# Kernel optimization log

Measured on AMD Instinct MI355X. Metric: run time of the kernel, lower is better.

Reference implementation:

```python
import jax, jax.numpy as jnp
import numpy as np

B, S, D = 2, 2048, 1024
H = 16
HD = D // H  # 64
SCALE = HD ** 0.5


def setup_inputs() -> dict:
    key = jax.random.key(0)
    ks = jax.random.split(key, 7)
    return {
        "query": jax.random.normal(ks[0], (B, S, D), dtype=jnp.float32),
        "key": jax.random.normal(ks[1], (B, S, D), dtype=jnp.float32),
        "value": jax.random.normal(ks[2], (B, S, D), dtype=jnp.float32),
        "W_qkv_w": jax.random.normal(ks[3], (3 * D, 3 * D), dtype=jnp.float32) * (1.0 / np.sqrt(3 * D)),
        "W_qkv_b": jax.random.normal(ks[4], (3 * D,), dtype=jnp.float32) * 0.02,
        "W_o_w": jax.random.normal(ks[5], (D, D), dtype=jnp.float32) * (1.0 / np.sqrt(D)),
        "W_o_b": jax.random.normal(ks[6], (D,), dtype=jnp.float32) * 0.02,
    }


def _split_heads(x):
    # [B,S,D] -> [B,H,S,HD]
    return x.reshape(B, S, H, HD).transpose(0, 2, 1, 3)


def reference(query, key, value, W_qkv_w, W_qkv_b, W_o_w, W_o_b):
    # fused QKV projection: concat then Linear(3D, 3D)  (torch: x @ W.T + b)
    qkv = jnp.concatenate([query, key, value], axis=-1)
    qkv = qkv @ W_qkv_w.T + W_qkv_b
    q, k, v = jnp.split(qkv, 3, axis=-1)
    q, k, v = _split_heads(q), _split_heads(k), _split_heads(v)
    # naive attention: materializes [B,H,S,S]
    scores = jnp.einsum('bhqd,bhkd->bhqk', q, k) / SCALE
    probs = jax.nn.softmax(scores, axis=-1)
    attn = jnp.einsum('bhqk,bhkd->bhqd', probs, v)
    # combine heads: [B,H,S,HD] -> [B,S,D]
    attn = attn.transpose(0, 2, 1, 3).reshape(B, S, D)
    return attn @ W_o_w.T + W_o_b
```

## Files before the change

kernel.cpp:

```cpp
#include <hip/hip_runtime.h>
#include <cmath>

#define BS   2
#define SEQ  2048
#define DM   1024
#define NH   16
#define HD   64
#define D3   3072
#define MROWS 4096
#define KVBLK 64
#define QBLK  128
#define NTILES (SEQ / KVBLK)

#define CSC 0.18033688011112042f

typedef _Float16 f16;
typedef __attribute__((ext_vector_type(4))) _Float16 half4;
typedef __attribute__((ext_vector_type(8))) _Float16 half8;
typedef __attribute__((ext_vector_type(4))) float f32x4;
typedef unsigned int u32;
typedef __attribute__((ext_vector_type(2))) u32 u32x2;
typedef __attribute__((ext_vector_type(4))) u32 u32x4;

__device__ __forceinline__ void async_cp16(const void* g, void* s) {
    __builtin_amdgcn_global_load_lds(
        (const __attribute__((address_space(1))) u32*)g,
        (__attribute__((address_space(3))) u32*)s, 16, 0, 0);
}

__global__ __launch_bounds__(256) void conv_concat_kernel(
    const float* __restrict__ q, const float* __restrict__ k,
    const float* __restrict__ v, f16* __restrict__ out)
{
    const int seg = blockIdx.x;
    const int row = blockIdx.y;
    const int c   = threadIdx.x * 4;
    const float* src = (seg == 0 ? q : (seg == 1 ? k : v)) + (size_t)row * DM + c;
    float4 x = *(const float4*)src;
    half4 h = {(f16)x.x, (f16)x.y, (f16)x.z, (f16)x.w};
    *(half4*)&out[(size_t)row * D3 + seg * DM + c] = h;
}

__global__ __launch_bounds__(256) void conv_plain_kernel(
    const float* __restrict__ src, f16* __restrict__ dst, int n4)
{
    int i = blockIdx.x * 256 + threadIdx.x;
    const int stride = gridDim.x * 256;
    for (; i < n4; i += stride) {
        float4 x = *(const float4*)&src[(size_t)i * 4];
        half4 h = {(f16)x.x, (f16)x.y, (f16)x.z, (f16)x.w};
        *(half4*)&dst[(size_t)i * 4] = h;
    }
}

template<int KDIM, int NDIM, bool F16OUT>
__global__ __launch_bounds__(256) void gemm_f16_kernel(
    const f16* __restrict__ A, const f16* __restrict__ W,
    const float* __restrict__ bias, void* __restrict__ Cout)
{
    __shared__ f16 As[128 * 32];
    __shared__ f16 Ws[128 * 32];

    const int tid  = threadIdx.x;
    const int lane = tid & 63;
    const int wave = tid >> 6;
    const int l15  = lane & 15;
    const int lg   = lane >> 4;
    const int wm   = wave >> 1;
    const int wn   = wave & 1;

    const int cpx = gridDim.x >> 3;
    const int lid = (blockIdx.x & 7) * cpx + (blockIdx.x >> 3);
    const int NT  = NDIM / 128;
    const int tM0 = (lid / NT) * 128;
    const int tN0 = (lid % NT) * 128;

    const int srow = lane >> 2;
    const int sch  = lane & 3;
    const int ssc  = sch ^ ((srow >> 1) & 3);

    const f16* gA0 = A + (size_t)(tM0 + wave * 32      + srow) * KDIM + ssc * 8;
    const f16* gA1 = A + (size_t)(tM0 + wave * 32 + 16 + srow) * KDIM + ssc * 8;
    const f16* gW0 = W + (size_t)(tN0 + wave * 32      + srow) * KDIM + ssc * 8;
    const f16* gW1 = W + (size_t)(tN0 + wave * 32 + 16 + srow) * KDIM + ssc * 8;
    f16* lA0 = &As[(wave * 32)      * 32];
    f16* lA1 = &As[(wave * 32 + 16) * 32];
    f16* lW0 = &Ws[(wave * 32)      * 32];
    f16* lW1 = &Ws[(wave * 32 + 16) * 32];

    f32x4 acc[4][4];
#pragma unroll
    for (int i = 0; i < 4; ++i)
#pragma unroll
        for (int j = 0; j < 4; ++j) acc[i][j] = (f32x4){0.f, 0.f, 0.f, 0.f};

    const int fsw = (lg ^ ((l15 >> 1) & 3)) * 8;
    int aoff[4], woff[4];
#pragma unroll
    for (int mi = 0; mi < 4; ++mi) aoff[mi] = (wm * 64 + mi * 16 + l15) * 32 + fsw;
#pragma unroll
    for (int ni = 0; ni < 4; ++ni) woff[ni] = (wn * 64 + ni * 16 + l15) * 32 + fsw;

    for (int k0 = 0; k0 < KDIM; k0 += 32) {
        __syncthreads();
        async_cp16(gA0 + k0, lA0);
        async_cp16(gA1 + k0, lA1);
        async_cp16(gW0 + k0, lW0);
        async_cp16(gW1 + k0, lW1);
        __syncthreads();

        half8 af[4], wf[4];
#pragma unroll
        for (int mi = 0; mi < 4; ++mi) af[mi] = *(half8*)&As[aoff[mi]];
#pragma unroll
        for (int ni = 0; ni < 4; ++ni) wf[ni] = *(half8*)&Ws[woff[ni]];
#pragma unroll
        for (int mi = 0; mi < 4; ++mi)
#pragma unroll
            for (int ni = 0; ni < 4; ++ni)
                acc[mi][ni] = __builtin_amdgcn_mfma_f32_16x16x32_f16(
                    af[mi], wf[ni], acc[mi][ni], 0, 0, 0);
    }

    float bv[4];
#pragma unroll
    for (int ni = 0; ni < 4; ++ni) bv[ni] = bias[tN0 + wn * 64 + ni * 16 + l15];

#pragma unroll
    for (int mi = 0; mi < 4; ++mi)
#pragma unroll
        for (int ni = 0; ni < 4; ++ni)
#pragma unroll
            for (int r = 0; r < 4; ++r) {
                const int m   = tM0 + wm * 64 + mi * 16 + lg * 4 + r;
                const int col = tN0 + wn * 64 + ni * 16 + l15;
                const float val = acc[mi][ni][r] + bv[ni];
                if constexpr (F16OUT)
                    ((f16*)Cout)[(size_t)m * NDIM + col] = (f16)val;
                else
                    ((float*)Cout)[(size_t)m * NDIM + col] = val;
            }
}


#define V_STORE(VtN, va, vb) do {                                             \
    u32x4 aw_ = __builtin_bit_cast(u32x4, va);                                \
    u32x4 bw_ = __builtin_bit_cast(u32x4, vb);                                \
    _Pragma("unroll")                                                         \
    for (int wd_ = 0; wd_ < 4; ++wd_) {                                       \
        u32 lo_ = __builtin_amdgcn_perm(bw_[wd_], aw_[wd_], 0x05040100u);     \
        u32 hi_ = __builtin_amdgcn_perm(bw_[wd_], aw_[wd_], 0x07060302u);     \
        const int dl_ = vd0 + 2 * wd_;                                        \
        const int dh_ = dl_ + 1;                                              \
        *(u32*)&VtN[dl_ * KVBLK + (((vp >> 2) ^ (dl_ & 7) ^ (dl_ >> 3)) * 8)  \
                    + 2 * (vp & 3)] = lo_;                                    \
        *(u32*)&VtN[dh_ * KVBLK + (((vp >> 2) ^ (dh_ & 7) ^ (dh_ >> 3)) * 8)  \
                    + 2 * (vp & 3)] = hi_;                                    \
    }                                                                         \
} while (0)

#define ATTN_STEP(KhC, VtC, KhN, VtN, TT, PF) do {                            \
    half8 va_ = {}, vb_ = {};                                                 \
    if (PF) {                                                                 \
        const size_t nro_ = (size_t)((TT) + 1) * KVBLK;                       \
        async_cp16(kxsrc + (nro_ + wave * 16 +     krow_l) * D3,              \
                   &KhN[(wave * 16) * HD]);                                   \
        async_cp16(kxsrc + (nro_ + wave * 16 + 8 + krow_l) * D3,              \
                   &KhN[(wave * 16 + 8) * HD]);                               \
        va_ = *(const half8*)(vsrc0 + nro_ * D3);                             \
        vb_ = *(const half8*)(vsrc0 + nro_ * D3 + D3);                        \
    }                                                                         \
    f32x4 sc[2][4];                                                           \
    _Pragma("unroll")                                                         \
    for (int rt = 0; rt < 2; ++rt)                                            \
        _Pragma("unroll")                                                     \
        for (int ct = 0; ct < 4; ++ct) sc[rt][ct] = (f32x4){0.f,0.f,0.f,0.f}; \
    __builtin_amdgcn_s_setprio(1);                                            \
    _Pragma("unroll")                                                         \
    for (int ct = 0; ct < 4; ++ct) {                                          \
        const int krow = ct * 16 + l15;                                       \
        _Pragma("unroll")                                                     \
        for (int ks = 0; ks < 2; ++ks) {                                      \
            half8 kf = *(half8*)&KhC[krow * HD +                              \
                                     (((ks * 4 + lg) ^ (krow & 7)) * 8)];     \
            _Pragma("unroll")                                                 \
            for (int rt = 0; rt < 2; ++rt)                                    \
                sc[rt][ct] = __builtin_amdgcn_mfma_f32_16x16x32_f16(          \
                    kf, qf[rt][ks], sc[rt][ct], 0, 0, 0);                     \
        }                                                                     \
    }                                                                         \
    __builtin_amdgcn_s_setprio(0);                                            \
    _Pragma("unroll")                                                         \
    for (int rt = 0; rt < 2; ++rt) {                                          \
        float mt = sc[rt][0][0];                                              \
        _Pragma("unroll")                                                     \
        for (int ct = 0; ct < 4; ++ct)                                        \
            _Pragma("unroll")                                                 \
            for (int r = 0; r < 4; ++r)                                       \
                if (ct || r) mt = fmaxf(mt, sc[rt][ct][r]);                   \
        mt = fmaxf(mt, __shfl_xor(mt, 16));                                   \
        mt = fmaxf(mt, __shfl_xor(mt, 32));                                   \
        const float mn = fmaxf(mrun[rt], mt * CSC);                           \
        const float alpha = exp2f(mrun[rt] - mn);                             \
        mrun[rt] = mn;                                                        \
        float pv_[4][4];                                                      \
        float ls = 0.f;                                                       \
        _Pragma("unroll")                                                     \
        for (int ct = 0; ct < 4; ++ct)                                        \
            _Pragma("unroll")                                                 \
            for (int r = 0; r < 4; ++r) {                                     \
                pv_[ct][r] = exp2f(fmaf(sc[rt][ct][r], CSC, -mn));            \
                ls += pv_[ct][r];                                             \
            }                                                                 \
        ls += __shfl_xor(ls, 16);                                             \
        ls += __shfl_xor(ls, 32);                                             \
        lrun[rt] = lrun[rt] * alpha + ls;                                     \
        _Pragma("unroll")                                                     \
        for (int dct = 0; dct < 4; ++dct)                                     \
            _Pragma("unroll")                                                 \
            for (int r = 0; r < 4; ++r) oacc[rt][dct][r] *= alpha;            \
        const int prow_ = pbase + (rt * 16 + l15) * KVBLK;                    \
        _Pragma("unroll")                                                     \
        for (int ct = 0; ct < 4; ++ct) {                                      \
            u32 w01 = __builtin_bit_cast(u32,                                 \
                __builtin_amdgcn_cvt_pkrtz(pv_[ct][0], pv_[ct][1]));          \
            u32 w23 = __builtin_bit_cast(u32,                                 \
                __builtin_amdgcn_cvt_pkrtz(pv_[ct][2], pv_[ct][3]));          \
            *(u32x2*)&Pl[prow_ + ((4 * ct + lg) ^ l15) * 4] =                 \
                (u32x2){w01, w23};                                            \
        }                                                                     \
    }                                                                         \
    __builtin_amdgcn_s_setprio(1);                                            \
    _Pragma("unroll")                                                         \
    for (int ks2 = 0; ks2 < 2; ++ks2) {                                       \
        half8 pa[2];                                                          \
        _Pragma("unroll")                                                     \
        for (int rt = 0; rt < 2; ++rt) {                                      \
            const int prow_ = pbase + (rt * 16 + l15) * KVBLK;                \
            half4 plA_ = *(half4*)&Pl[prow_ + ((8 * ks2 + 2 * lg)     ^ l15) * 4]; \
            half4 plB_ = *(half4*)&Pl[prow_ + ((8 * ks2 + 2 * lg + 1) ^ l15) * 4]; \
            pa[rt] = __builtin_shufflevector(plA_, plB_, 0,1,2,3,4,5,6,7);    \
        }                                                                     \
        _Pragma("unroll")                                                     \
        for (int dct = 0; dct < 4; ++dct) {                                   \
            const int d = dct * 16 + l15;                                     \
            half8 vf = *(half8*)&VtC[d * KVBLK +                              \
                        (((ks2 * 4 + lg) ^ (d & 7) ^ (d >> 3)) * 8)];         \
            _Pragma("unroll")                                                 \
            for (int rt = 0; rt < 2; ++rt)                                    \
                oacc[rt][dct] = __builtin_amdgcn_mfma_f32_16x16x32_f16(       \
                    vf, pa[rt], oacc[rt][dct], 0, 0, 0);                      \
        }                                                                     \
    }                                                                         \
    __builtin_amdgcn_s_setprio(0);                                            \
    if (PF) { V_STORE(VtN, va_, vb_); }                                       \
    __syncthreads();                                                          \
} while (0)

__global__ __launch_bounds__(256, 2) void attn_mfma_kernel(
    const f16* __restrict__ qkvh, f16* __restrict__ attnh)
{
    __shared__ f16 Kh0[KVBLK * HD];
    __shared__ f16 Kh1[KVBLK * HD];
    __shared__ f16 Vt0[HD * KVBLK];
    __shared__ f16 Vt1[HD * KVBLK];
    __shared__ f16 Pl[4 * 32 * KVBLK];

    const int tid  = threadIdx.x;
    const int lane = tid & 63;
    const int wave = tid >> 6;
    const int l15  = lane & 15;
    const int lg   = lane >> 4;

    const int nq  = SEQ / QBLK;
    const int cpx = gridDim.x >> 3;
    const int lid = (blockIdx.x & 7) * cpx + (blockIdx.x >> 3);
    const int b   = lid / (NH * nq);
    const int h   = (lid / nq) % NH;
    const int qc  = lid % nq;
    const int q0  = qc * QBLK + wave * 32;
    const size_t bS = (size_t)b * SEQ;

    const int krow_l = lane >> 3;
    const int kschk  = (lane & 7) ^ krow_l;
    const f16* kxsrc = qkvh + bS * D3 + DM + h * HD + kschk * 8;

    const int vp  = tid >> 3;
    const int vd0 = (tid & 7) * 8;
    const f16* vsrc0 = qkvh + (bS + 2 * vp) * D3 + 2 * DM + h * HD + vd0;

    half8 qf[2][2];
#pragma unroll
    for (int rt = 0; rt < 2; ++rt)
#pragma unroll
        for (int ks = 0; ks < 2; ++ks)
            qf[rt][ks] = *(const half8*)&qkvh[(bS + q0 + rt * 16 + l15) * D3 +
                                              h * HD + ks * 32 + lg * 8];

    f32x4 oacc[2][4];
#pragma unroll
    for (int rt = 0; rt < 2; ++rt)
#pragma unroll
        for (int dct = 0; dct < 4; ++dct) oacc[rt][dct] = (f32x4){0.f, 0.f, 0.f, 0.f};

    float mrun[2], lrun[2];
#pragma unroll
    for (int rt = 0; rt < 2; ++rt) { mrun[rt] = -INFINITY; lrun[rt] = 0.f; }

    const int pbase = wave * 32 * KVBLK;

    {
        async_cp16(kxsrc + (size_t)(wave * 16 +     krow_l) * D3, &Kh0[(wave * 16) * HD]);
        async_cp16(kxsrc + (size_t)(wave * 16 + 8 + krow_l) * D3, &Kh0[(wave * 16 + 8) * HD]);
        half8 va_ = *(const half8*)(vsrc0);
        half8 vb_ = *(const half8*)(vsrc0 + D3);
        V_STORE(Vt0, va_, vb_);
        __syncthreads();
    }

    for (int t = 0; t < NTILES; t += 2) {
        ATTN_STEP(Kh0, Vt0, Kh1, Vt1, t, true);
        ATTN_STEP(Kh1, Vt1, Kh0, Vt0, t + 1, (t + 1) < (NTILES - 1));
    }

#pragma unroll
    for (int rt = 0; rt < 2; ++rt) {
        const float inv = 1.f / lrun[rt];
        const int qq = q0 + rt * 16 + l15;
#pragma unroll
        for (int dct = 0; dct < 4; ++dct) {
            half4 o;
#pragma unroll
            for (int r = 0; r < 4; ++r) o[r] = (f16)(oacc[rt][dct][r] * inv);
            *(half4*)&attnh[(bS + qq) * DM + h * HD + dct * 16 + 4 * lg] = o;
        }
    }
}

extern "C" void kernel_launch(void* const* d_in, const int* in_sizes, int n_in,
                              void* d_out, int out_size, void* d_ws, size_t ws_size,
                              hipStream_t stream) {
    const float* q    = (const float*)d_in[0];
    const float* k    = (const float*)d_in[1];
    const float* v    = (const float*)d_in[2];
    const float* Wqkv = (const float*)d_in[3];
    const float* bqkv = (const float*)d_in[4];
    const float* Wo   = (const float*)d_in[5];
    const float* bo   = (const float*)d_in[6];
    float* out = (float*)d_out;

    char* ws = (char*)d_ws;
    f16* Ain    = (f16*)ws;
    f16* attn_h = (f16*)ws;
    f16* Wo_h   = (f16*)(ws + 16777216);
    f16* Wqkv_h = (f16*)(ws + 25165824);
    f16* qkv_h  = (f16*)(ws + 44040192);

    conv_concat_kernel<<<dim3(3, MROWS), 256, 0, stream>>>(q, k, v, Ain);
    conv_plain_kernel<<<2048, 256, 0, stream>>>(Wqkv, Wqkv_h, D3 * D3 / 4);

    gemm_f16_kernel<D3, D3, true><<<dim3((MROWS / 128) * (D3 / 128)), 256, 0, stream>>>(
        Ain, Wqkv_h, bqkv, qkv_h);

    attn_mfma_kernel<<<dim3(BS * NH * (SEQ / QBLK)), 256, 0, stream>>>(qkv_h, attn_h);

    conv_plain_kernel<<<512, 256, 0, stream>>>(Wo, Wo_h, DM * DM / 4);

    gemm_f16_kernel<DM, DM, false><<<dim3((MROWS / 128) * (DM / 128)), 256, 0, stream>>>(
        attn_h, Wo_h, bo, out);
}
```

Baseline: 215.7 us.

## Deepen GEMM K-tile, halve attention Q-block, add lazy softmax rescaling

New measurement: 229.3 us. +6.3%, slower.

```diff
diff --git a/kernel.cpp b/kernel.cpp
--- a/kernel.cpp
+++ b/kernel.cpp
@@ -9,7 +9,7 @@
 #define D3   3072
 #define MROWS 4096
 #define KVBLK 64
-#define QBLK  128
+#define QBLK  64
 #define NTILES (SEQ / KVBLK)
 
 #define CSC 0.18033688011112042f
@@ -53,13 +53,24 @@
     }
 }
 
+#define GSTAGE(K0) do {                                                       \
+    async_cp16(gA + (K0),                 lA);                                \
+    async_cp16(gA + (K0) +  8 * KDIM,     lA +  8 * 64);                      \
+    async_cp16(gA + (K0) + 16 * KDIM,     lA + 16 * 64);                      \
+    async_cp16(gA + (K0) + 24 * KDIM,     lA + 24 * 64);                      \
+    async_cp16(gW + (K0),                 lW);                                \
+    async_cp16(gW + (K0) +  8 * KDIM,     lW +  8 * 64);                      \
+    async_cp16(gW + (K0) + 16 * KDIM,     lW + 16 * 64);                      \
+    async_cp16(gW + (K0) + 24 * KDIM,     lW + 24 * 64);                      \
+} while (0)
+
 template<int KDIM, int NDIM, bool F16OUT>
 __global__ __launch_bounds__(256) void gemm_f16_kernel(
     const f16* __restrict__ A, const f16* __restrict__ W,
     const float* __restrict__ bias, void* __restrict__ Cout)
 {
-    __shared__ f16 As[128 * 32];
-    __shared__ f16 Ws[128 * 32];
+    __shared__ f16 As[128 * 64];
+    __shared__ f16 Ws[128 * 64];
 
     const int tid  = threadIdx.x;
     const int lane = tid & 63;
@@ -71,22 +82,17 @@
 
     const int cpx = gridDim.x >> 3;
     const int lid = (blockIdx.x & 7) * cpx + (blockIdx.x >> 3);
-    const int NT  = NDIM / 128;
-    const int tM0 = (lid / NT) * 128;
-    const int tN0 = (lid % NT) * 128;
-
-    const int srow = lane >> 2;
-    const int sch  = lane & 3;
-    const int ssc  = sch ^ ((srow >> 1) & 3);
-
-    const f16* gA0 = A + (size_t)(tM0 + wave * 32      + srow) * KDIM + ssc * 8;
-    const f16* gA1 = A + (size_t)(tM0 + wave * 32 + 16 + srow) * KDIM + ssc * 8;
-    const f16* gW0 = W + (size_t)(tN0 + wave * 32      + srow) * KDIM + ssc * 8;
-    const f16* gW1 = W + (size_t)(tN0 + wave * 32 + 16 + srow) * KDIM + ssc * 8;
-    f16* lA0 = &As[(wave * 32)      * 32];
-    f16* lA1 = &As[(wave * 32 + 16) * 32];
-    f16* lW0 = &Ws[(wave * 32)      * 32];
-    f16* lW1 = &Ws[(wave * 32 + 16) * 32];
+    const int NT2 = NDIM / 128;
+    const int tM0 = (lid / NT2) * 128;
+    const int tN0 = (lid % NT2) * 128;
+
+    const int r8  = lane >> 3;
+    const int ssc = (lane & 7) ^ r8;
+
+    const f16* gA = A + (size_t)(tM0 + wave * 32 + r8) * KDIM + ssc * 8;
+    const f16* gW = W + (size_t)(tN0 + wave * 32 + r8) * KDIM + ssc * 8;
+    f16* lA = &As[(wave * 32) * 64];
+    f16* lW = &Ws[(wave * 32) * 64];
 
     f32x4 acc[4][4];
 #pragma unroll
@@ -94,32 +100,35 @@
 #pragma unroll
         for (int j = 0; j < 4; ++j) acc[i][j] = (f32x4){0.f, 0.f, 0.f, 0.f};
 
-    const int fsw = (lg ^ ((l15 >> 1) & 3)) * 8;
+    const int h7 = l15 & 7;
     int aoff[4], woff[4];
 #pragma unroll
-    for (int mi = 0; mi < 4; ++mi) aoff[mi] = (wm * 64 + mi * 16 + l15) * 32 + fsw;
-#pragma unroll
-    for (int ni = 0; ni < 4; ++ni) woff[ni] = (wn * 64 + ni * 16 + l15) * 32 + fsw;
-
-    for (int k0 = 0; k0 < KDIM; k0 += 32) {
+    for (int mi = 0; mi < 4; ++mi) aoff[mi] = (wm * 64 + mi * 16 + l15) * 64;
+#pragma unroll
+    for (int ni = 0; ni < 4; ++ni) woff[ni] = (wn * 64 + ni * 16 + l15) * 64;
+    const int csw0 = (lg ^ h7) * 8;
+    const int csw1 = ((4 + lg) ^ h7) * 8;
+
+    for (int k0 = 0; k0 < KDIM; k0 += 64) {
         __syncthreads();
-        async_cp16(gA0 + k0, lA0);
-        async_cp16(gA1 + k0, lA1);
-        async_cp16(gW0 + k0, lW0);
-        async_cp16(gW1 + k0, lW1);
+        GSTAGE(k0);
         __syncthreads();
 
-        half8 af[4], wf[4];
-#pragma unroll
-        for (int mi = 0; mi < 4; ++mi) af[mi] = *(half8*)&As[aoff[mi]];
-#pragma unroll
-        for (int ni = 0; ni < 4; ++ni) wf[ni] = *(half8*)&Ws[woff[ni]];
-#pragma unroll
-        for (int mi = 0; mi < 4; ++mi)
-#pragma unroll
-            for (int ni = 0; ni < 4; ++ni)
-                acc[mi][ni] = __builtin_amdgcn_mfma_f32_16x16x32_f16(
-                    af[mi], wf[ni], acc[mi][ni], 0, 0, 0);
+#pragma unroll
+        for (int ks = 0; ks < 2; ++ks) {
+            const int csw = ks ? csw1 : csw0;
+            half8 af[4], wf[4];
+#pragma unroll
+            for (int mi = 0; mi < 4; ++mi) af[mi] = *(half8*)&As[aoff[mi] + csw];
+#pragma unroll
+            for (int ni = 0; ni < 4; ++ni) wf[ni] = *(half8*)&Ws[woff[ni] + csw];
+#pragma unroll
+            for (int mi = 0; mi < 4; ++mi)
+#pragma unroll
+                for (int ni = 0; ni < 4; ++ni)
+                    acc[mi][ni] = __builtin_amdgcn_mfma_f32_16x16x32_f16(
+                        af[mi], wf[ni], acc[mi][ni], 0, 0, 0);
+        }
     }
 
     float bv[4];
@@ -143,7 +152,7 @@
 }
 
 
-#define V_STORE(VtN, va, vb) do {                                             \
+#define V_STORE2(VtN, va, vb, vpx) do {                                       \
     u32x4 aw_ = __builtin_bit_cast(u32x4, va);                                \
     u32x4 bw_ = __builtin_bit_cast(u32x4, vb);                                \
     _Pragma("unroll")                                                         \
@@ -152,23 +161,29 @@
         u32 hi_ = __builtin_amdgcn_perm(bw_[wd_], aw_[wd_], 0x07060302u);     \
         const int dl_ = vd0 + 2 * wd_;                                        \
         const int dh_ = dl_ + 1;                                              \
-        *(u32*)&VtN[dl_ * KVBLK + (((vp >> 2) ^ (dl_ & 7) ^ (dl_ >> 3)) * 8)  \
-                    + 2 * (vp & 3)] = lo_;                                    \
-        *(u32*)&VtN[dh_ * KVBLK + (((vp >> 2) ^ (dh_ & 7) ^ (dh_ >> 3)) * 8)  \
-                    + 2 * (vp & 3)] = hi_;                                    \
+        *(u32*)&VtN[dl_ * KVBLK + ((((vpx) >> 2) ^ (dl_ & 7) ^ (dl_ >> 3)) * 8) \
+                    + 2 * ((vpx) & 3)] = lo_;                                 \
+        *(u32*)&VtN[dh_ * KVBLK + ((((vpx) >> 2) ^ (dh_ & 7) ^ (dh_ >> 3)) * 8) \
+                    + 2 * ((vpx) & 3)] = hi_;                                 \
     }                                                                         \
 } while (0)
 
 #define ATTN_STEP(KhC, VtC, KhN, VtN, TT, PF) do {                            \
-    half8 va_ = {}, vb_ = {};                                                 \
+    half8 va_ = {}, vb_ = {}, vc_ = {}, vd_ = {};                             \
     if (PF) {                                                                 \
         const size_t nro_ = (size_t)((TT) + 1) * KVBLK;                       \
-        async_cp16(kxsrc + (nro_ + wave * 16 +     krow_l) * D3,              \
-                   &KhN[(wave * 16) * HD]);                                   \
-        async_cp16(kxsrc + (nro_ + wave * 16 + 8 + krow_l) * D3,              \
-                   &KhN[(wave * 16 + 8) * HD]);                               \
+        async_cp16(kxsrc + (nro_ + wave * 32 +      krow_l) * D3,             \
+                   &KhN[(wave * 32) * HD]);                                   \
+        async_cp16(kxsrc + (nro_ + wave * 32 +  8 + krow_l) * D3,             \
+                   &KhN[(wave * 32 + 8) * HD]);                               \
+        async_cp16(kxsrc + (nro_ + wave * 32 + 16 + krow_l) * D3,             \
+                   &KhN[(wave * 32 + 16) * HD]);                              \
+        async_cp16(kxsrc + (nro_ + wave * 32 + 24 + krow_l) * D3,             \
+                   &KhN[(wave * 32 + 24) * HD]);                              \
         va_ = *(const half8*)(vsrc0 + nro_ * D3);                             \
         vb_ = *(const half8*)(vsrc0 + nro_ * D3 + D3);                        \
+        vc_ = *(const half8*)(vsrc0 + (nro_ + 32) * D3);                      \
+        vd_ = *(const half8*)(vsrc0 + (nro_ + 33) * D3);                      \
     }                                                                         \
     f32x4 sc[2][4];                                                           \
     _Pragma("unroll")                                                         \
@@ -192,33 +207,41 @@
     __builtin_amdgcn_s_setprio(0);                                            \
     _Pragma("unroll")                                                         \
     for (int rt = 0; rt < 2; ++rt) {                                          \
-        float mt = sc[rt][0][0];                                              \
-        _Pragma("unroll")                                                     \
-        for (int ct = 0; ct < 4; ++ct)                                        \
-            _Pragma("unroll")                                                 \
-            for (int r = 0; r < 4; ++r)                                       \
-                if (ct || r) mt = fmaxf(mt, sc[rt][ct][r]);                   \
+        float mA_ = fmaxf(fmaxf(sc[rt][0][0], sc[rt][0][1]),                  \
+                          fmaxf(sc[rt][0][2], sc[rt][0][3]));                 \
+        float mB_ = fmaxf(fmaxf(sc[rt][1][0], sc[rt][1][1]),                  \
+                          fmaxf(sc[rt][1][2], sc[rt][1][3]));                 \
+        float mC_ = fmaxf(fmaxf(sc[rt][2][0], sc[rt][2][1]),                  \
+                          fmaxf(sc[rt][2][2], sc[rt][2][3]));                 \
+        float mD_ = fmaxf(fmaxf(sc[rt][3][0], sc[rt][3][1]),                  \
+                          fmaxf(sc[rt][3][2], sc[rt][3][3]));                 \
+        float mt = fmaxf(fmaxf(mA_, mB_), fmaxf(mC_, mD_));                   \
         mt = fmaxf(mt, __shfl_xor(mt, 16));                                   \
         mt = fmaxf(mt, __shfl_xor(mt, 32));                                   \
-        const float mn = fmaxf(mrun[rt], mt * CSC);                           \
-        const float alpha = exp2f(mrun[rt] - mn);                             \
-        mrun[rt] = mn;                                                        \
+        const float mtc = mt * CSC;                                           \
+        if (__any(mtc - mrun[rt] > 8.0f)) {                                   \
+            const float mn = fmaxf(mrun[rt], mtc);                            \
+            const float alpha = exp2f(mrun[rt] - mn);                         \
+            mrun[rt] = mn;                                                    \
+            lrun[rt] *= alpha;                                                \
+            _Pragma("unroll")                                                 \
+            for (int dct = 0; dct < 4; ++dct)                                 \
+                _Pragma("unroll")                                             \
+                for (int r = 0; r < 4; ++r) oacc[rt][dct][r] *= alpha;        \
+        }                                                                     \
+        const float mn_ = mrun[rt];                                           \
         float pv_[4][4];                                                      \
         float ls = 0.f;                                                       \
         _Pragma("unroll")                                                     \
         for (int ct = 0; ct < 4; ++ct)                                        \
             _Pragma("unroll")                                                 \
             for (int r = 0; r < 4; ++r) {                                     \
-                pv_[ct][r] = exp2f(fmaf(sc[rt][ct][r], CSC, -mn));            \
+                pv_[ct][r] = exp2f(fmaf(sc[rt][ct][r], CSC, -mn_));           \
                 ls += pv_[ct][r];                                             \
             }                                                                 \
         ls += __shfl_xor(ls, 16);                                             \
         ls += __shfl_xor(ls, 32);                                             \
-        lrun[rt] = lrun[rt] * alpha + ls;                                     \
-        _Pragma("unroll")                                                     \
-        for (int dct = 0; dct < 4; ++dct)                                     \
-            _Pragma("unroll")                                                 \
-            for (int r = 0; r < 4; ++r) oacc[rt][dct][r] *= alpha;            \
+        lrun[rt] += ls;                                                       \
         const int prow_ = pbase + (rt * 16 + l15) * KVBLK;                    \
         _Pragma("unroll")                                                     \
         for (int ct = 0; ct < 4; ++ct) {                                      \
@@ -253,18 +276,18 @@
         }                                                                     \
     }                                                                         \
     __builtin_amdgcn_s_setprio(0);                                            \
-    if (PF) { V_STORE(VtN, va_, vb_); }                                       \
+    if (PF) { V_STORE2(VtN, va_, vb_, vp); V_STORE2(VtN, vc_, vd_, vp + 16); }\
     __syncthreads();                                                          \
 } while (0)
 
-__global__ __launch_bounds__(256, 2) void attn_mfma_kernel(
+__global__ __launch_bounds__(128, 2) void attn_mfma_kernel(
     const f16* __restrict__ qkvh, f16* __restrict__ attnh)
 {
     __shared__ f16 Kh0[KVBLK * HD];
     __shared__ f16 Kh1[KVBLK * HD];
     __shared__ f16 Vt0[HD * KVBLK];
     __shared__ f16 Vt1[HD * KVBLK];
-    __shared__ f16 Pl[4 * 32 * KVBLK];
+    __shared__ f16 Pl[2 * 32 * KVBLK];
 
     const int tid  = threadIdx.x;
     const int lane = tid & 63;
@@ -310,11 +333,16 @@
     const int pbase = wave * 32 * KVBLK;
 
     {
-        async_cp16(kxsrc + (size_t)(wave * 16 +     krow_l) * D3, &Kh0[(wave * 16) * HD]);
-        async_cp16(kxsrc + (size_t)(wave * 16 + 8 + krow_l) * D3, &Kh0[(wave * 16 + 8) * HD]);
+        async_cp16(kxsrc + (size_t)(wave * 32 +      krow_l) * D3, &Kh0[(wave * 32) * HD]);
+        async_cp16(kxsrc + (size_t)(wave * 32 +  8 + krow_l) * D3, &Kh0[(wave * 32 + 8) * HD]);
+        async_cp16(kxsrc + (size_t)(wave * 32 + 16 + krow_l) * D3, &Kh0[(wave * 32 + 16) * HD]);
+        async_cp16(kxsrc + (size_t)(wave * 32 + 24 + krow_l) * D3, &Kh0[(wave * 32 + 24) * HD]);
         half8 va_ = *(const half8*)(vsrc0);
         half8 vb_ = *(const half8*)(vsrc0 + D3);
-        V_STORE(Vt0, va_, vb_);
+        half8 vc_ = *(const half8*)(vsrc0 + 32 * D3);
+        half8 vd_ = *(const half8*)(vsrc0 + 33 * D3);
+        V_STORE2(Vt0, va_, vb_, vp);
+        V_STORE2(Vt0, vc_, vd_, vp + 16);
         __syncthreads();
     }
 
@@ -362,7 +390,7 @@
     gemm_f16_kernel<D3, D3, true><<<dim3((MROWS / 128) * (D3 / 128)), 256, 0, stream>>>(
         Ain, Wqkv_h, bqkv, qkv_h);
 
-    attn_mfma_kernel<<<dim3(BS * NH * (SEQ / QBLK)), 256, 0, stream>>>(qkv_h, attn_h);
+    attn_mfma_kernel<<<dim3(BS * NH * (SEQ / QBLK)), 128, 0, stream>>>(qkv_h, attn_h);
 
     conv_plain_kernel<<<512, 256, 0, stream>>>(Wo, Wo_h, DM * DM / 4);
 
```
